# Optimization experiments

Hardware: AMD Instinct MI355X
Metric: run time of the kernel (lower is better)

## Reference

```python
import jax, jax.numpy as jnp
import numpy as np

K_RADIUS = 1            # 2k+1 = 3 neighborhood -> 9 offsets
AFF_THRESH = 0.5        # affinity = 1/(1+dist); edge iff affinity > 0.5 (dist < 1)
N_PROP_STEPS = 40       # label propagation iterations
M_PARENTS = 256         # max parent segments per image (num_nodes of next level)


def _offsets(k):
    return [(dy, dx) for dy in range(-k, k + 1) for dx in range(-k, k + 1)]


def _shift2d(x, dy, dx, fill):
    """Shift spatial dims (axes 1,2) of x by (dy,dx), padding with `fill`."""
    kr = K_RADIUS
    pad = [(0, 0), (kr, kr), (kr, kr)] + [(0, 0)] * (x.ndim - 3)
    xp = jnp.pad(x, pad, constant_values=fill)
    H, W = x.shape[1], x.shape[2]
    return xp[:, kr + dy:kr + dy + H, kr + dx:kr + dx + W]


def setup_inputs() -> dict:
    key = jax.random.key(0)
    features = jax.random.normal(key, (32, 128, 128, 64), dtype=jnp.float32)
    return {"features": features}


def reference(features):
    BT, H, W, C = features.shape
    N = H * W
    offs = _offsets(K_RADIUS)

    # ---- compute_affinities: inverse Euclidean distance in (2k+1)^2 window ----
    aff_list = []
    for dy, dx in offs:
        nb = _shift2d(features, dy, dx, fill=1e6)  # out-of-bounds -> huge dist -> aff ~ 0
        dist = jnp.sqrt(jnp.sum((features - nb) ** 2, axis=-1) + 1e-12)
        aff_list.append(1.0 / (1.0 + dist))
    affinities = jnp.stack(aff_list, axis=-1)      # [BT,H,W,K]

    # ---- threshold_affinities ----
    edges = affinities > AFF_THRESH                # [BT,H,W,K] bool

    # ---- compute_parents: label propagation (min-label flooding over edges) ----
    labels0 = jnp.broadcast_to(
        jnp.arange(N, dtype=jnp.int32).reshape(1, H, W), (BT, H, W))
    SENT = jnp.int32(N)  # sentinel larger than any label

    def body(_, lab):
        cands = [lab]
        for j, (dy, dx) in enumerate(offs):
            nb = _shift2d(lab, dy, dx, fill=N)
            cands.append(jnp.where(edges[..., j], nb, SENT))
        return jnp.min(jnp.stack(cands, axis=0), axis=0)

    labels = jax.lax.fori_loop(0, N_PROP_STEPS, body, labels0)  # [BT,H,W]
    lab_flat = labels.reshape(BT, N)

    # ---- register_parents: relabel to contiguous ids, capped at M (preproc_segment_ids) ----
    def relabel(lab):
        present = jnp.zeros((N,), jnp.int32).at[lab].set(1)
        rank = jnp.cumsum(present) - 1
        return jnp.minimum(rank[lab], M_PARENTS - 1)

    seg = jax.vmap(relabel)(lab_flat)              # [BT,N] in [0,M)

    # ---- aggregate_nodes_and_features: per-segment mean and variance ----
    flat_ids = (seg + jnp.arange(BT, dtype=jnp.int32)[:, None] * M_PARENTS).reshape(-1)
    feat = features.reshape(BT * N, C)
    sums = jax.ops.segment_sum(feat, flat_ids, num_segments=BT * M_PARENTS)
    sqs = jax.ops.segment_sum(feat * feat, flat_ids, num_segments=BT * M_PARENTS)
    cnt = jax.ops.segment_sum(jnp.ones((BT * N, 1), feat.dtype), flat_ids,
                              num_segments=BT * M_PARENTS)
    denom = jnp.maximum(cnt, 1.0)
    mean = sums / denom
    var = jnp.maximum(sqs / denom - mean * mean, 0.0)
    parent_nodes = jnp.concatenate([mean, var], axis=-1).reshape(BT, M_PARENTS, 2 * C)
    return parent_nodes
```

## Files before the change

kernel.cpp:

```cpp
#include <hip/hip_runtime.h>
#include <stdint.h>

#define HH 128
#define WW 128
#define NPIX 16384
#define BTN 32
#define CCH 64
#define MPAR 256
#define SENT 16384
#define NSTEPS 40

#define ETX 32
#define ETY 8
__global__ __launch_bounds__(256) void edge_kernel(const float* __restrict__ feat,
                                                   unsigned char* __restrict__ mask4,
                                                   float4* __restrict__ accz,
                                                   float4* __restrict__ cntz) {
  __shared__ float lds[8][308];
  int blk = blockIdx.x;
  int tid = threadIdx.x;

  if (tid < 128) accz[blk * 128 + tid] = make_float4(0.f, 0.f, 0.f, 0.f);
  else if (tid == 128) cntz[blk] = make_float4(0.f, 0.f, 0.f, 0.f);

  int b = blk >> 6;
  int t = blk & 63;
  int ty0 = (t >> 2) * ETY;
  int tx0 = (t & 3) * ETX;
  const float* fb = feat + ((size_t)b << 20);

  for (int sp = tid; sp < 306; sp += 256) {
    int gy = ty0 + sp / 34;
    int gx = tx0 - 1 + sp % 34;
    if (gy < HH && (unsigned)gx < (unsigned)WW) {
      const float* pp = fb + (((size_t)(gy << 7) + gx) << 6);
      float4 v0 = *(const float4*)pp;
      float4 v1 = *(const float4*)(pp + 4);
      lds[0][sp] = v0.x; lds[1][sp] = v0.y; lds[2][sp] = v0.z; lds[3][sp] = v0.w;
      lds[4][sp] = v1.x; lds[5][sp] = v1.y; lds[6][sp] = v1.z; lds[7][sp] = v1.w;
    } else {
#pragma unroll
      for (int c = 0; c < 8; ++c) lds[c][sp] = 1e6f;
    }
  }
  __syncthreads();

  int tx = tid & 31, ty = tid >> 5;
  int idx = ty * 34 + tx + 1;
  int gx = tx0 + tx, gy = ty0 + ty;

  float own[8];
#pragma unroll
  for (int c = 0; c < 8; ++c) own[c] = lds[c][idx];
  float a0 = 0.f, a1 = 0.f, a2 = 0.f, a3 = 0.f;
#pragma unroll
  for (int c = 0; c < 8; ++c) {
    float o = own[c];
    float d0 = o - lds[c][idx + 1];
    float d1 = o - lds[c][idx + 33];
    float d2 = o - lds[c][idx + 34];
    float d3 = o - lds[c][idx + 35];
    a0 += d0 * d0; a1 += d1 * d1; a2 += d2 * d2; a3 += d3 * d3;
  }

  bool vS = (gy + 1) < HH;
  float acc[4] = {a0, a1, a2, a3};
  bool val[4] = {(gx + 1) < WW, vS && gx >= 1, vS, vS && (gx + 1) < WW};
  const int offp[4] = {1, 127, 128, 129};
  const float* fp = fb + (((size_t)(gy << 7) + gx) << 6);
  unsigned m = 0;
#pragma unroll
  for (int j = 0; j < 4; ++j) {
    if (val[j]) {
      float s = acc[j];
      if (s < 1.0f) {
        const float* np_ = fp + ((size_t)offp[j] << 6);
        for (int c = 8; c < 64; ++c) {
          float d = fp[c] - np_[c];
          s += d * d;
        }
      }
      if (s + 1e-12f < 1.0f) m |= (1u << j);
    }
  }
  mask4[(b << 14) + (gy << 7) + gx] = (unsigned char)m;
}

__global__ __launch_bounds__(1024) void prop_kernel(const unsigned char* __restrict__ mask4g,
                                                    unsigned char* __restrict__ segg) {
  __shared__ __align__(16) unsigned short lab[NPIX];
  __shared__ __align__(16) unsigned char e8[NPIX];
  __shared__ __align__(16) unsigned short rnk[NPIX];
  __shared__ int flags[2];
  __shared__ int wsum[16];
  __shared__ int wexc[16];
  __shared__ int wany[16];
  int b = blockIdx.x;
  int tid = threadIdx.x;
  int lane = tid & 63, wid = tid >> 6;

  uint4 mv = ((const uint4*)(mask4g + ((size_t)b << 14)))[tid];
  ((uint4*)e8)[tid] = mv;
  unsigned anyv = mv.x | mv.y | mv.z | mv.w;
  unsigned long long bal = __ballot(anyv != 0);
  if (lane == 0) wany[wid] = (bal != 0ull) ? 1 : 0;
  __syncthreads();

  int tot = 0;
#pragma unroll
  for (int i = 0; i < 16; ++i) tot |= wany[i];
  if (tot == 0) {
    uint4 w;
    if (tid < 16) {
      unsigned b0 = (unsigned)(tid * 16);
      w.x = b0 | ((b0 + 1) << 8) | ((b0 + 2) << 16) | ((b0 + 3) << 24);
      w.y = (b0 + 4) | ((b0 + 5) << 8) | ((b0 + 6) << 16) | ((b0 + 7) << 24);
      w.z = (b0 + 8) | ((b0 + 9) << 8) | ((b0 + 10) << 16) | ((b0 + 11) << 24);
      w.w = (b0 + 12) | ((b0 + 13) << 8) | ((b0 + 14) << 16) | ((b0 + 15) << 24);
    } else {
      w = make_uint4(~0u, ~0u, ~0u, ~0u);
    }
    ((uint4*)(segg + ((size_t)b << 14)))[tid] = w;
    return;
  }

  unsigned char tmp[16];
  {
    int base = tid * 16;
#pragma unroll
    for (int i = 0; i < 16; ++i) {
      int p = base + i;
      int y = p >> 7, x = p & (WW - 1);
      unsigned own = e8[p];
      unsigned nw = (y > 0 && x > 0) ? e8[p - 129] : 0;
      unsigned n_ = (y > 0) ? e8[p - 128] : 0;
      unsigned ne = (y > 0 && x < WW - 1) ? e8[p - 127] : 0;
      unsigned w_ = (x > 0) ? e8[p - 1] : 0;
      unsigned v = ((nw >> 3) & 1) | (((n_ >> 2) & 1) << 1) | (((ne >> 1) & 1) << 2) |
                   ((w_ & 1) << 3) | ((own & 1) << 4) | (((own >> 1) & 1) << 5) |
                   (((own >> 2) & 1) << 6) | (((own >> 3) & 1) << 7);
      tmp[i] = (unsigned char)v;
    }
  }
  __syncthreads();
  {
    int base = tid * 16;
#pragma unroll
    for (int i = 0; i < 16; ++i) e8[base + i] = tmp[i];
#pragma unroll
    for (int i = 0; i < 16; ++i) lab[base + i] = (unsigned short)(base + i);
  }
  if (tid == 0) { flags[0] = 0; flags[1] = 0; }
  __syncthreads();

  int x0 = (tid & 31) * 4, y0 = (tid >> 5) * 4;
  int cur[4][4], eb[4][4];
#pragma unroll
  for (int r = 0; r < 4; ++r)
#pragma unroll
    for (int c = 0; c < 4; ++c) {
      cur[r][c] = (y0 + r) * WW + x0 + c;
      eb[r][c] = e8[(y0 + r) * WW + x0 + c];
    }

  for (int it = 0; it < NSTEPS; ++it) {
    int top[6], bot[6], lft[4], rgt[4];
#pragma unroll
    for (int c = 0; c < 6; ++c) {
      top[c] = lab[(((y0 - 1) * WW) + x0 - 1 + c) & (NPIX - 1)];
      bot[c] = lab[(((y0 + 4) * WW) + x0 - 1 + c) & (NPIX - 1)];
    }
#pragma unroll
    for (int r = 0; r < 4; ++r) {
      lft[r] = lab[(((y0 + r) * WW) + x0 - 1) & (NPIX - 1)];
      rgt[r] = lab[(((y0 + r) * WW) + x0 + 4) & (NPIX - 1)];
    }
    int nl[4][4];
    bool ch = false;
#pragma unroll
    for (int r = 0; r < 4; ++r) {
#pragma unroll
      for (int c = 0; c < 4; ++c) {
        int m = cur[r][c];
        int e = eb[r][c];
        int v;
        v = (r > 0) ? ((c > 0) ? cur[r - 1][c - 1] : lft[r - 1]) : top[c];
        m = min(m, (e & 1) ? v : SENT);
        v = (r > 0) ? cur[r - 1][c] : top[c + 1];
        m = min(m, (e & 2) ? v : SENT);
        v = (r > 0) ? ((c < 3) ? cur[r - 1][c + 1] : rgt[r - 1]) : top[c + 2];
        m = min(m, (e & 4) ? v : SENT);
        v = (c > 0) ? cur[r][c - 1] : lft[r];
        m = min(m, (e & 8) ? v : SENT);
        v = (c < 3) ? cur[r][c + 1] : rgt[r];
        m = min(m, (e & 16) ? v : SENT);
        v = (r < 3) ? ((c > 0) ? cur[r + 1][c - 1] : lft[r + 1]) : bot[c];
        m = min(m, (e & 32) ? v : SENT);
        v = (r < 3) ? cur[r + 1][c] : bot[c + 1];
        m = min(m, (e & 64) ? v : SENT);
        v = (r < 3) ? ((c < 3) ? cur[r + 1][c + 1] : rgt[r + 1]) : bot[c + 2];
        m = min(m, (e & 128) ? v : SENT);
        nl[r][c] = m;
        ch |= (m != cur[r][c]);
      }
    }
    __syncthreads();
#pragma unroll
    for (int r = 0; r < 4; ++r) {
      unsigned lo = (unsigned)nl[r][0] | ((unsigned)nl[r][1] << 16);
      unsigned hi = (unsigned)nl[r][2] | ((unsigned)nl[r][3] << 16);
      *((uint2*)&lab[(y0 + r) * WW + x0]) = make_uint2(lo, hi);
    }
    if (ch) flags[it & 1] = 1;
    if (tid == 0) flags[(it + 1) & 1] = 0;
#pragma unroll
    for (int r = 0; r < 4; ++r)
#pragma unroll
      for (int c = 0; c < 4; ++c) cur[r][c] = nl[r][c];
    __syncthreads();
    if (!flags[it & 1]) break;
  }

  __syncthreads();
  ((uint4*)e8)[tid] = make_uint4(0u, 0u, 0u, 0u);
  __syncthreads();
#pragma unroll
  for (int i = 0; i < 16; ++i) {
    int p = tid + i * 1024;
    e8[lab[p]] = 1;
  }
  __syncthreads();
  int pres[16];
  int base = tid * 16;
#pragma unroll
  for (int i = 0; i < 16; ++i) pres[i] = e8[base + i];
  int s_local = 0;
#pragma unroll
  for (int i = 0; i < 16; ++i) s_local += pres[i];
  int inc = s_local;
#pragma unroll
  for (int off = 1; off < 64; off <<= 1) {
    int v = __shfl_up(inc, off, 64);
    if (lane >= off) inc += v;
  }
  if (lane == 63) wsum[wid] = inc;
  __syncthreads();
  if (wid == 0) {
    int tt = (lane < 16) ? wsum[lane] : 0;
    int winc = tt;
#pragma unroll
    for (int off = 1; off < 16; off <<= 1) {
      int v = __shfl_up(winc, off, 64);
      if (lane >= off) winc += v;
    }
    if (lane < 16) wexc[lane] = winc - tt;
  }
  __syncthreads();
  int run = wexc[wid] + (inc - s_local);
#pragma unroll
  for (int i = 0; i < 16; ++i) {
    run += pres[i];
    rnk[base + i] = (unsigned short)(run - 1);
  }
  __syncthreads();
  unsigned char* so = segg + ((size_t)b << 14);
#pragma unroll
  for (int i = 0; i < 16; ++i) {
    int p = tid + i * 1024;
    int sg = rnk[lab[p]];
    so[p] = (unsigned char)min(sg, 255);
  }
}

#define PXW 128
__global__ __launch_bounds__(256) void agg_kernel(const float* __restrict__ feat,
                                                  const unsigned char* __restrict__ segg,
                                                  float* __restrict__ acc,
                                                  float* __restrict__ cnt) {
  __shared__ float xb[4][128];
  int lane = threadIdx.x & 63;
  int wid = threadIdx.x >> 6;
  int gw = blockIdx.x * 4 + wid;
  int b = gw >> 7;
  int chunk = gw & 127;
  int basep = (b << 14) + (chunk << 7);
  const unsigned char* sp = segg + basep;
  int s0 = sp[lane];
  int s1 = sp[64 + lane];
  int c0 = __builtin_amdgcn_readfirstlane(s0);

  if (__all(s0 == c0 && s1 == c0)) {
    const float4* fq = (const float4*)(feat + ((size_t)basep << 6));
    int phase = lane >> 4, q = lane & 15;
    float4 s4 = make_float4(0.f, 0.f, 0.f, 0.f);
    float4 q4 = make_float4(0.f, 0.f, 0.f, 0.f);
#pragma unroll
    for (int i = 0; i < 32; ++i) {
      float4 v = fq[(size_t)i * 64 + (size_t)phase * 16 + q];
      s4.x += v.x; s4.y += v.y; s4.z += v.z; s4.w += v.w;
      q4.x += v.x * v.x; q4.y += v.y * v.y; q4.z += v.z * v.z; q4.w += v.w * v.w;
    }
#pragma unroll
    for (int off = 16; off < 64; off <<= 1) {
      s4.x += __shfl_xor(s4.x, off); s4.y += __shfl_xor(s4.y, off);
      s4.z += __shfl_xor(s4.z, off); s4.w += __shfl_xor(s4.w, off);
      q4.x += __shfl_xor(q4.x, off); q4.y += __shfl_xor(q4.y, off);
      q4.z += __shfl_xor(q4.z, off); q4.w += __shfl_xor(q4.w, off);
    }
    if (phase == 0) *((float4*)&xb[wid][q * 4]) = s4;
    else if (phase == 1) *((float4*)&xb[wid][64 + q * 4]) = q4;
    float sacc = xb[wid][lane];
    float qacc = xb[wid][64 + lane];
    float* a = acc + ((size_t)((b << 8) + c0) << 7);
    atomicAdd(a + lane, sacc);
    atomicAdd(a + 64 + lane, qacc);
    if (lane == 0) atomicAdd(cnt + (b << 8) + c0, 128.0f);
    return;
  }

  const float* fp = feat + ((size_t)basep << 6) + lane;
  float sacc = 0.f, qacc = 0.f, cacc = 0.f;
  int curs = c0;

  float v[32];
#pragma unroll
  for (int u = 0; u < 32; ++u) v[u] = fp[(size_t)u << 6];

#pragma unroll
  for (int kk = 0; kk < PXW; kk += 32) {
    float w[32];
    if (kk + 32 < PXW) {
#pragma unroll
      for (int u = 0; u < 32; ++u) w[u] = fp[(size_t)(kk + 32 + u) << 6];
    }
#pragma unroll
    for (int u = 0; u < 32; ++u) {
      int k = kk + u;
      int sg = __builtin_amdgcn_readlane((k & 64) ? s1 : s0, k & 63);
      if (sg != curs) {
        float* a = acc + ((size_t)((b << 8) + curs) << 7);
        atomicAdd(a + lane, sacc);
        atomicAdd(a + 64 + lane, qacc);
        if (lane == 0) atomicAdd(cnt + (b << 8) + curs, cacc);
        curs = sg; sacc = 0.f; qacc = 0.f; cacc = 0.f;
      }
      sacc += v[u]; qacc += v[u] * v[u]; cacc += 1.f;
    }
#pragma unroll
    for (int u = 0; u < 32; ++u) v[u] = w[u];
  }
  {
    float* a = acc + ((size_t)((b << 8) + curs) << 7);
    atomicAdd(a + lane, sacc);
    atomicAdd(a + 64 + lane, qacc);
    if (lane == 0) atomicAdd(cnt + (b << 8) + curs, cacc);
  }
}

__global__ __launch_bounds__(256) void fin_kernel(float* __restrict__ acc,
                                                  const float* __restrict__ cnt) {
  int gid = blockIdx.x * 256 + threadIdx.x;
  int bm = gid >> 6, c = gid & 63;
  float* a = acc + ((size_t)bm << 7);
  float s = a[c], q = a[c + 64];
  float n = cnt[bm];
  float denom = fmaxf(n, 1.0f);
  float mean = s / denom;
  float var = fmaxf(q / denom - mean * mean, 0.0f);
  a[c] = mean;
  a[c + 64] = var;
}

extern "C" void kernel_launch(void* const* d_in, const int* in_sizes, int n_in,
                              void* d_out, int out_size, void* d_ws, size_t ws_size,
                              hipStream_t stream) {
  const float* feat = (const float*)d_in[0];
  unsigned char* mask4 = (unsigned char*)d_ws;
  unsigned char* segg = mask4 + (size_t)BTN * NPIX;
  float* cnt = (float*)(segg + (size_t)BTN * NPIX);
  float* acc = (float*)d_out;

  edge_kernel<<<BTN * 64, 256, 0, stream>>>(feat, mask4, (float4*)acc, (float4*)cnt);
  prop_kernel<<<BTN, 1024, 0, stream>>>(mask4, segg);
  agg_kernel<<<BTN * NPIX / PXW / 4, 256, 0, stream>>>(feat, segg, acc, cnt);
  fin_kernel<<<BTN * MPAR * CCH / 256, 256, 0, stream>>>(acc, cnt);
}
```

Measured before the change: 219.3 us.

## Replace uniform-chunk atomics with per-wave partials reduced in finalize kernel

When a 128-pixel chunk belongs to a single segment, the aggregation kernel now writes its partial sums, squares, segment id and count to per-wave workspace slots instead of issuing global atomics into the accumulator. The finalize kernel scans the 128 wave partials of each image, adds those that match the segment, then folds in the atomic accumulator for non-uniform chunks and writes to a separate output buffer. This targets contention on the few heavily shared segment accumulators, at the cost of a 128-entry scan per output element in the finalize step.

```diff
diff --git a/kernel.cpp b/kernel.cpp
--- a/kernel.cpp
+++ b/kernel.cpp
@@ -9,6 +9,8 @@
 #define MPAR 256
 #define SENT 16384
 #define NSTEPS 40
+#define PXW 128
+#define NWAVE (BTN * NPIX / PXW)
 
 #define ETX 32
 #define ETY 8
@@ -272,12 +274,14 @@
   }
 }
 
-#define PXW 128
 __global__ __launch_bounds__(256) void agg_kernel(const float* __restrict__ feat,
                                                   const unsigned char* __restrict__ segg,
                                                   float* __restrict__ acc,
-                                                  float* __restrict__ cnt) {
-  __shared__ float xb[4][128];
+                                                  float* __restrict__ cnt,
+                                                  float* __restrict__ psum,
+                                                  float* __restrict__ psq,
+                                                  int* __restrict__ pseg,
+                                                  float* __restrict__ pcnt) {
   int lane = threadIdx.x & 63;
   int wid = threadIdx.x >> 6;
   int gw = blockIdx.x * 4 + wid;
@@ -307,17 +311,13 @@
       q4.x += __shfl_xor(q4.x, off); q4.y += __shfl_xor(q4.y, off);
       q4.z += __shfl_xor(q4.z, off); q4.w += __shfl_xor(q4.w, off);
     }
-    if (phase == 0) *((float4*)&xb[wid][q * 4]) = s4;
-    else if (phase == 1) *((float4*)&xb[wid][64 + q * 4]) = q4;
-    float sacc = xb[wid][lane];
-    float qacc = xb[wid][64 + lane];
-    float* a = acc + ((size_t)((b << 8) + c0) << 7);
-    atomicAdd(a + lane, sacc);
-    atomicAdd(a + 64 + lane, qacc);
-    if (lane == 0) atomicAdd(cnt + (b << 8) + c0, 128.0f);
+    if (phase == 0) *(float4*)(psum + ((size_t)gw << 6) + (q << 2)) = s4;
+    else if (phase == 1) *(float4*)(psq + ((size_t)gw << 6) + (q << 2)) = q4;
+    if (lane == 0) { pseg[gw] = c0; pcnt[gw] = 128.0f; }
     return;
   }
 
+  if (lane == 0) pseg[gw] = -1;
   const float* fp = feat + ((size_t)basep << 6) + lane;
   float sacc = 0.f, qacc = 0.f, cacc = 0.f;
   int curs = c0;
@@ -357,18 +357,36 @@
   }
 }
 
-__global__ __launch_bounds__(256) void fin_kernel(float* __restrict__ acc,
-                                                  const float* __restrict__ cnt) {
+__global__ __launch_bounds__(256) void fin_kernel(const float* __restrict__ psum,
+                                                  const float* __restrict__ psq,
+                                                  const int* __restrict__ pseg,
+                                                  const float* __restrict__ pcnt,
+                                                  const float* __restrict__ acc,
+                                                  const float* __restrict__ cnt,
+                                                  float* __restrict__ out) {
   int gid = blockIdx.x * 256 + threadIdx.x;
   int bm = gid >> 6, c = gid & 63;
-  float* a = acc + ((size_t)bm << 7);
-  float s = a[c], q = a[c + 64];
-  float n = cnt[bm];
+  int bmu = __builtin_amdgcn_readfirstlane(bm);
+  int b = bmu >> 8, m = bmu & 255;
+  int wbase = b << 7;
+  float s = 0.f, q = 0.f, n = 0.f;
+  for (int w = 0; w < 128; ++w) {
+    if (pseg[wbase + w] == m) {
+      s += psum[((size_t)(wbase + w) << 6) + c];
+      q += psq[((size_t)(wbase + w) << 6) + c];
+      n += pcnt[wbase + w];
+    }
+  }
+  const float* a = acc + ((size_t)bmu << 7);
+  s += a[c];
+  q += a[c + 64];
+  n += cnt[bmu];
   float denom = fmaxf(n, 1.0f);
   float mean = s / denom;
   float var = fmaxf(q / denom - mean * mean, 0.0f);
-  a[c] = mean;
-  a[c + 64] = var;
+  float* o = out + ((size_t)bmu << 7);
+  o[c] = mean;
+  o[c + 64] = var;
 }
 
 extern "C" void kernel_launch(void* const* d_in, const int* in_sizes, int n_in,
@@ -378,10 +396,15 @@
   unsigned char* mask4 = (unsigned char*)d_ws;
   unsigned char* segg = mask4 + (size_t)BTN * NPIX;
   float* cnt = (float*)(segg + (size_t)BTN * NPIX);
-  float* acc = (float*)d_out;
+  float* acc = cnt + (size_t)BTN * MPAR;
+  float* psum = acc + (size_t)BTN * MPAR * 128;
+  float* psq = psum + (size_t)NWAVE * 64;
+  float* pcnt = psq + (size_t)NWAVE * 64;
+  int* pseg = (int*)(pcnt + NWAVE);
+  float* out = (float*)d_out;
 
   edge_kernel<<<BTN * 64, 256, 0, stream>>>(feat, mask4, (float4*)acc, (float4*)cnt);
   prop_kernel<<<BTN, 1024, 0, stream>>>(mask4, segg);
-  agg_kernel<<<BTN * NPIX / PXW / 4, 256, 0, stream>>>(feat, segg, acc, cnt);
-  fin_kernel<<<BTN * MPAR * CCH / 256, 256, 0, stream>>>(acc, cnt);
+  agg_kernel<<<NWAVE / 4, 256, 0, stream>>>(feat, segg, acc, cnt, psum, psq, pseg, pcnt);
+  fin_kernel<<<BTN * MPAR * CCH / 256, 256, 0, stream>>>(psum, psq, pseg, pcnt, acc, cnt, out);
 }
```

New measurement: 258.0 us. +17.7%, slower.
